# Kernel tuning notes

Measured on AMD Instinct MI355X. Metric: run time of the kernel, lower is better.

The kernel has to match this reference:

```python
import jax, jax.numpy as jnp
import numpy as np

BN_EPS = 1e-5

def _bn_eval(x, g, b, m, v):
    # BatchNorm1d in eval mode with running stats
    return (x - m) * (g / jnp.sqrt(v + BN_EPS)) + b

def _gcn_layer(x, adj, w, b):
    # D^-0.5 A D^-0.5 (X W) + b  (same math as diag(d^-0.5) @ adj @ diag(d^-0.5))
    deg = adj.sum(axis=1)
    dis = deg ** -0.5
    xw = x @ w
    return dis[:, None] * (adj @ (dis[:, None] * xw)) + b

def setup_inputs() -> dict:
    key = jax.random.key(0)
    ks = jax.random.split(key, 8)
    N, F, E, H, G, C = 16384, 1024, 256, 256, 128, 10
    def xavier(k, i, o):
        s = float(np.sqrt(6.0 / (i + o)))
        return jax.random.uniform(k, (i, o), jnp.float32, -s, s)
    return {
        "feature": jax.random.uniform(ks[0], (N, F), jnp.float32),
        "adj": jax.random.uniform(ks[1], (N, N), jnp.float32),
        "enc_w1": xavier(ks[2], F, 512), "enc_b1": jnp.zeros((512,), jnp.float32),
        "bn1_g": jnp.ones((512,), jnp.float32), "bn1_b": jnp.zeros((512,), jnp.float32),
        "bn1_m": jnp.zeros((512,), jnp.float32), "bn1_v": jnp.ones((512,), jnp.float32),
        "enc_w2": xavier(ks[3], 512, E), "enc_b2": jnp.zeros((E,), jnp.float32),
        "bn2_g": jnp.ones((E,), jnp.float32), "bn2_b": jnp.zeros((E,), jnp.float32),
        "bn2_m": jnp.zeros((E,), jnp.float32), "bn2_v": jnp.ones((E,), jnp.float32),
        "gcn1_w": xavier(ks[4], E, H), "gcn1_b": jnp.zeros((H,), jnp.float32),
        "gcn2_w": xavier(ks[5], H, G), "gcn2_b": jnp.zeros((G,), jnp.float32),
        "cls_w": xavier(ks[6], G, C), "cls_b": jnp.zeros((C,), jnp.float32),
    }

def reference(feature, adj, enc_w1, enc_b1, bn1_g, bn1_b, bn1_m, bn1_v,
              enc_w2, enc_b2, bn2_g, bn2_b, bn2_m, bn2_v,
              gcn1_w, gcn1_b, gcn2_w, gcn2_b, cls_w, cls_b):
    # encoder.encode (eval: dropout off, BN running stats)
    h = jax.nn.relu(_bn_eval(feature @ enc_w1 + enc_b1, bn1_g, bn1_b, bn1_m, bn1_v))
    h = jax.nn.relu(_bn_eval(h @ enc_w2 + enc_b2, bn2_g, bn2_b, bn2_m, bn2_v))
    h = jax.nn.relu(_gcn_layer(h, adj, gcn1_w, gcn1_b))
    h = jax.nn.relu(_gcn_layer(h, adj, gcn2_w, gcn2_b))
    out = jax.nn.sigmoid(h @ cls_w + cls_b)
    return jnp.clip(out, 1e-10, 1 - 1e-10)
```

## Files before the change

### kernel.cpp

```cpp
#include <hip/hip_runtime.h>
#include <stdint.h>

typedef unsigned short u16;
typedef unsigned int u32;
typedef __attribute__((ext_vector_type(4))) float f32x4;
typedef __attribute__((ext_vector_type(16))) float f32x16;
typedef __attribute__((ext_vector_type(8))) short s16x8;
typedef __attribute__((ext_vector_type(4))) short s16x4;
typedef __attribute__((ext_vector_type(2))) unsigned int u32x2;
typedef __attribute__((ext_vector_type(4))) unsigned int u32x4;
typedef __attribute__((ext_vector_type(8))) int i32x8;

__device__ __forceinline__ u16 f2bf(float x){
  unsigned u = __builtin_bit_cast(unsigned, x);
  u += 0x7fffu + ((u >> 16) & 1u);
  return (u16)(u >> 16);
}
__device__ __forceinline__ float bf2f(u16 b){
  return __builtin_bit_cast(float, (unsigned)b << 16);
}
__device__ __forceinline__ u32 pk_fp8x4(float a, float b, float c, float d){
  int w = 0;
  w = __builtin_amdgcn_cvt_pk_fp8_f32(a, b, w, false);
  w = __builtin_amdgcn_cvt_pk_fp8_f32(c, d, w, true);
  return (u32)w;
}


__device__ __forceinline__ void tcvtT_dev(const float* __restrict__ src, u16* __restrict__ dst,
                                          int K, int N, int bx, int by, char* smem){
  float (*t)[33] = (float (*)[33])smem;
  int tx = threadIdx.x & 31, ty = threadIdx.x >> 5;
  int n0 = bx * 32, k0 = by * 32;
  #pragma unroll
  for (int i = 0; i < 4; i++)
    t[ty + 8 * i][tx] = src[(size_t)(k0 + ty + 8 * i) * N + n0 + tx];
  __syncthreads();
  #pragma unroll
  for (int i = 0; i < 4; i++)
    dst[(size_t)(n0 + ty + 8 * i) * K + k0 + tx] = f2bf(t[tx][ty + 8 * i]);
}

__device__ __forceinline__ void bn_dev(const float* __restrict__ g, const float* __restrict__ b,
                                       const float* __restrict__ m, const float* __restrict__ v,
                                       const float* __restrict__ lin_b,
                                       float* __restrict__ s, float* __restrict__ bb,
                                       int n, int blk){
  int i = blk * 256 + threadIdx.x;
  if (i < n){
    float sc = g[i] * rsqrtf(v[i] + 1e-5f);
    s[i] = sc;
    bb[i] = (lin_b[i] - m[i]) * sc + b[i];
  }
}

__global__ __launch_bounds__(256) void prep0_kernel(
    const float* __restrict__ enc_w1, u16* __restrict__ w1t,
    const float* __restrict__ g, const float* __restrict__ b,
    const float* __restrict__ m, const float* __restrict__ v,
    const float* __restrict__ lin_b, float* __restrict__ s1, float* __restrict__ bb1)
{
  __shared__ char smem[32 * 33 * 4 + 64];
  if (blockIdx.x < 512)
    tcvtT_dev(enc_w1, w1t, 1024, 512, blockIdx.x & 15, blockIdx.x >> 4, smem);
  else
    bn_dev(g, b, m, v, lin_b, s1, bb1, 512, blockIdx.x - 512);
}

__global__ __launch_bounds__(256) void enc1_deg_kernel(
    const float* __restrict__ feature, const u16* __restrict__ w1t,
    u16* __restrict__ h1, const float* __restrict__ cs, const float* __restrict__ cb,
    const float* __restrict__ adj, unsigned char* __restrict__ adj8,
    float* __restrict__ dis,
    const float* __restrict__ enc_w2, u16* __restrict__ w2t,
    const float* __restrict__ gcn1_w, u16* __restrict__ g1t,
    const float* __restrict__ gcn2_w, u16* __restrict__ g2t,
    const float* __restrict__ bn2_g, const float* __restrict__ bn2_b,
    const float* __restrict__ bn2_m, const float* __restrict__ bn2_v,
    const float* __restrict__ enc_b2, float* __restrict__ s2, float* __restrict__ bb2)
{
  constexpr int BM = 128, BN = 256, BK = 64, WM = 2, WN = 2;
  constexpr int N = 512, K = 1024, NADJ = 16384;
  constexpr int WTM = BM / WM, WTN = BN / WN, FM = WTM / 16, FN = WTN / 16;
  constexpr int AIT = (BM * BK) / (256 * 4);
  constexpr int BIT = (BN * BK) / (256 * 8);

  __shared__ __align__(16) char smem[BM * BK * 2 + BN * BK * 2];

  if (blockIdx.x >= 16640){
    int p = blockIdx.x - 16640;
    if (p < 128)       tcvtT_dev(enc_w2, w2t, 512, 256, p & 7, p >> 3, smem);
    else if (p < 192){ int l = p - 128; tcvtT_dev(gcn1_w, g1t, 256, 256, l & 7, l >> 3, smem); }
    else if (p < 224){ int l = p - 192; tcvtT_dev(gcn2_w, g2t, 256, 128, l & 3, l >> 2, smem); }
    else               bn_dev(bn2_g, bn2_b, bn2_m, bn2_v, enc_b2, s2, bb2, 256, 0);
    return;
  }

  if (blockIdx.x >= 256){
    int row = blockIdx.x - 256;
    const float* rp = adj + (size_t)row * NADJ;
    unsigned char* wp = adj8 + (size_t)row * NADJ;
    float s = 0.f;
    #pragma unroll
    for (int it = 0; it < 4; ++it){
      const float* p = rp + it * 4096 + threadIdx.x * 16;
      f32x4 v[4];
      #pragma unroll
      for (int j = 0; j < 4; ++j) v[j] = *(const f32x4*)(p + 4 * j);
      u32x4 o;
      #pragma unroll
      for (int j = 0; j < 4; ++j){
        s += (v[j][0] + v[j][1]) + (v[j][2] + v[j][3]);
        o[j] = pk_fp8x4(v[j][0], v[j][1], v[j][2], v[j][3]);
      }
      *(u32x4*)(wp + it * 4096 + threadIdx.x * 16) = o;
    }
    #pragma unroll
    for (int d = 32; d > 0; d >>= 1) s += __shfl_down(s, d, 64);
    float* ps = (float*)smem;
    if ((threadIdx.x & 63) == 0) ps[threadIdx.x >> 6] = s;
    __syncthreads();
    if (threadIdx.x == 0) dis[row] = rsqrtf((ps[0] + ps[1]) + (ps[2] + ps[3]));
    return;
  }

  u16* As = (u16*)smem;
  u16* Bs = (u16*)(smem + BM * BK * 2);
  const int tid = threadIdx.x;
  const int lane = tid & 63;
  const int wid = tid >> 6;
  const int wr = wid / WN;
  const int wc = wid % WN;
  const int bm = (blockIdx.x & 127) * BM;
  const int bn = (blockIdx.x >> 7) * BN;

  f32x4 arf[AIT];
  s16x8 brb[BIT];

  auto load_tiles = [&](int k0){
    #pragma unroll
    for (int i = 0; i < AIT; i++){
      int e = (i * 256 + tid) * 4; int r = e / BK, c = e % BK;
      arf[i] = *(const f32x4*)(feature + (size_t)(bm + r) * K + k0 + c);
    }
    #pragma unroll
    for (int i = 0; i < BIT; i++){
      int e = (i * 256 + tid) * 8; int r = e / BK, c = e % BK;
      brb[i] = *(const s16x8*)(w1t + (size_t)(bn + r) * K + k0 + c);
    }
  };
  auto store_tiles = [&](){
    char* Ac = (char*)As; char* Bc = (char*)Bs;
    #pragma unroll
    for (int i = 0; i < AIT; i++){
      int e = (i * 256 + tid) * 4; int r = e / BK, c = e % BK;
      int off = ((r * BK + c) * 2) ^ ((r & 7) << 4);
      s16x4 o;
      o[0] = (short)f2bf(arf[i][0]); o[1] = (short)f2bf(arf[i][1]);
      o[2] = (short)f2bf(arf[i][2]); o[3] = (short)f2bf(arf[i][3]);
      *(s16x4*)(Ac + off) = o;
    }
    #pragma unroll
    for (int i = 0; i < BIT; i++){
      int e = (i * 256 + tid) * 8; int r = e / BK, c = e % BK;
      int off = ((r * BK + c) * 2) ^ ((r & 7) << 4);
      *(s16x8*)(Bc + off) = brb[i];
    }
  };

  f32x4 acc[FM][FN];
  #pragma unroll
  for (int m = 0; m < FM; m++)
    #pragma unroll
    for (int n = 0; n < FN; n++)
      acc[m][n] = (f32x4){0.f, 0.f, 0.f, 0.f};

  const int arow0 = wr * WTM + (lane & 15);
  const int brow0 = wc * WTN + (lane & 15);
  const int kof = (lane >> 4) * 8;

  load_tiles(0);
  for (int kt = 0; kt < K / BK; ++kt){
    __syncthreads();
    store_tiles();
    __syncthreads();
    if (kt + 1 < K / BK) load_tiles((kt + 1) * BK);
    const char* Ac = (const char*)As;
    const char* Bc = (const char*)Bs;
    #pragma unroll
    for (int ks = 0; ks < BK / 32; ++ks){
      s16x8 af[FM], bfr[FN];
      #pragma unroll
      for (int m = 0; m < FM; m++){
        int r = arow0 + m * 16;
        af[m] = *(const s16x8*)(Ac + (((r * BK + ks * 32 + kof) * 2) ^ ((r & 7) << 4)));
      }
      #pragma unroll
      for (int n = 0; n < FN; n++){
        int r = brow0 + n * 16;
        bfr[n] = *(const s16x8*)(Bc + (((r * BK + ks * 32 + kof) * 2) ^ ((r & 7) << 4)));
      }
      #pragma unroll
      for (int m = 0; m < FM; m++)
        #pragma unroll
        for (int n = 0; n < FN; n++)
          acc[m][n] = __builtin_amdgcn_mfma_f32_16x16x32_bf16(af[m], bfr[n], acc[m][n], 0, 0, 0);
    }
  }
  #pragma unroll
  for (int m = 0; m < FM; m++){
    #pragma unroll
    for (int n = 0; n < FN; n++){
      int col = bn + wc * WTN + n * 16 + (lane & 15);
      int row0 = bm + wr * WTM + m * 16 + (lane >> 4) * 4;
      #pragma unroll
      for (int r4 = 0; r4 < 4; r4++){
        float vv = fmaxf(acc[m][n][r4] * cs[col] + cb[col], 0.f);
        h1[(size_t)(row0 + r4) * N + col] = f2bf(vv);
      }
    }
  }
}

__global__ __launch_bounds__(512, 1)
void h2tT_kernel(const u16* __restrict__ h1, const u16* __restrict__ w2t,
                 const float* __restrict__ s2, const float* __restrict__ bb2,
                 const u16* __restrict__ g1t, const float* __restrict__ dis,
                 unsigned char* __restrict__ tT)
{
  constexpr int M = 16384, K1 = 512, K2 = 256, BK = 128;
  constexpr float SC = 256.f;

  __shared__ u16 As[64 * BK];
  __shared__ u16 Bs[256 * BK];
  __shared__ u16 H2s[64 * 256];

  const int tid = threadIdx.x;
  const int lane = tid & 63;
  const int wid = tid >> 6;
  const int wr = wid >> 2;
  const int wc = wid & 3;
  const int bm = blockIdx.x * 64;
  const int kof = (lane >> 4) * 8;

  {
    s16x8 arb[2], brb[8];
    auto load1 = [&](int k0){
      #pragma unroll
      for (int i = 0; i < 2; i++){
        int e = (i * 512 + tid) * 8; int r = e >> 7, c = e & 127;
        arb[i] = *(const s16x8*)(h1 + (size_t)(bm + r) * K1 + k0 + c);
      }
      #pragma unroll
      for (int i = 0; i < 8; i++){
        int e = (i * 512 + tid) * 8; int r = e >> 7, c = e & 127;
        brb[i] = *(const s16x8*)(w2t + (size_t)r * K1 + k0 + c);
      }
    };
    auto store1 = [&](){
      char* Ac = (char*)As; char* Bc = (char*)Bs;
      #pragma unroll
      for (int i = 0; i < 2; i++){
        int e = (i * 512 + tid) * 8; int r = e >> 7, c = e & 127;
        *(s16x8*)(Ac + (((r * BK + c) * 2) ^ ((r & 7) << 4))) = arb[i];
      }
      #pragma unroll
      for (int i = 0; i < 8; i++){
        int e = (i * 512 + tid) * 8; int r = e >> 7, c = e & 127;
        *(s16x8*)(Bc + (((r * BK + c) * 2) ^ ((r & 7) << 4))) = brb[i];
      }
    };

    f32x4 acc[2][4];
    #pragma unroll
    for (int m = 0; m < 2; m++)
      #pragma unroll
      for (int n = 0; n < 4; n++)
        acc[m][n] = (f32x4){0.f, 0.f, 0.f, 0.f};

    load1(0);
    for (int kt = 0; kt < K1 / BK; ++kt){
      __syncthreads();
      store1();
      __syncthreads();
      if (kt + 1 < K1 / BK) load1((kt + 1) * BK);
      const char* Ac = (const char*)As;
      const char* Bc = (const char*)Bs;
      #pragma unroll
      for (int ks = 0; ks < 4; ++ks){
        s16x8 af[2], bfr[4];
        #pragma unroll
        for (int m = 0; m < 2; m++){
          int r = wr * 32 + m * 16 + (lane & 15);
          af[m] = *(const s16x8*)(Ac + (((r * BK + ks * 32 + kof) * 2) ^ ((r & 7) << 4)));
        }
        #pragma unroll
        for (int n = 0; n < 4; n++){
          int r = wc * 64 + n * 16 + (lane & 15);
          bfr[n] = *(const s16x8*)(Bc + (((r * BK + ks * 32 + kof) * 2) ^ ((r & 7) << 4)));
        }
        #pragma unroll
        for (int m = 0; m < 2; m++)
          #pragma unroll
          for (int n = 0; n < 4; n++)
            acc[m][n] = __builtin_amdgcn_mfma_f32_16x16x32_bf16(af[m], bfr[n], acc[m][n], 0, 0, 0);
      }
    }
    __syncthreads();
    char* Hc = (char*)H2s;
    #pragma unroll
    for (int m = 0; m < 2; m++){
      #pragma unroll
      for (int n = 0; n < 4; n++){
        int col = wc * 64 + n * 16 + (lane & 15);
        int row0 = wr * 32 + m * 16 + (lane >> 4) * 4;
        #pragma unroll
        for (int r4 = 0; r4 < 4; r4++){
          int row = row0 + r4;
          float vv = fmaxf(acc[m][n][r4] * s2[col] + bb2[col], 0.f);
          *(u16*)(Hc + (((row * 256 + col) * 2) ^ ((row & 7) << 4))) = f2bf(vv);
        }
      }
    }
  }

  {
    s16x8 brb[8];
    auto load2 = [&](int k0){
      #pragma unroll
      for (int i = 0; i < 8; i++){
        int e = (i * 512 + tid) * 8; int r = e >> 7, c = e & 127;
        brb[i] = *(const s16x8*)(g1t + (size_t)r * K2 + k0 + c);
      }
    };
    auto store2 = [&](){
      char* Bc = (char*)Bs;
      #pragma unroll
      for (int i = 0; i < 8; i++){
        int e = (i * 512 + tid) * 8; int r = e >> 7, c = e & 127;
        *(s16x8*)(Bc + (((r * BK + c) * 2) ^ ((r & 7) << 4))) = brb[i];
      }
    };

    f32x4 acc[2][4];
    #pragma unroll
    for (int m = 0; m < 2; m++)
      #pragma unroll
      for (int n = 0; n < 4; n++)
        acc[m][n] = (f32x4){0.f, 0.f, 0.f, 0.f};

    load2(0);
    for (int kt = 0; kt < K2 / BK; ++kt){
      __syncthreads();
      store2();
      __syncthreads();
      if (kt + 1 < K2 / BK) load2((kt + 1) * BK);
      const char* Hc = (const char*)H2s;
      const char* Bc = (const char*)Bs;
      #pragma unroll
      for (int ks = 0; ks < 4; ++ks){
        s16x8 af[2], bfr[4];
        #pragma unroll
        for (int m = 0; m < 2; m++){
          int r = wr * 32 + m * 16 + (lane & 15);
          af[m] = *(const s16x8*)(Hc + (((r * 256 + kt * 128 + ks * 32 + kof) * 2) ^ ((r & 7) << 4)));
        }
        #pragma unroll
        for (int n = 0; n < 4; n++){
          int r = wc * 64 + n * 16 + (lane & 15);
          bfr[n] = *(const s16x8*)(Bc + (((r * BK + ks * 32 + kof) * 2) ^ ((r & 7) << 4)));
        }
        #pragma unroll
        for (int m = 0; m < 2; m++)
          #pragma unroll
          for (int n = 0; n < 4; n++)
            acc[m][n] = __builtin_amdgcn_mfma_f32_16x16x32_bf16(af[m], bfr[n], acc[m][n], 0, 0, 0);
      }
    }
    #pragma unroll
    for (int m = 0; m < 2; m++){
      #pragma unroll
      for (int n = 0; n < 4; n++){
        int col = wc * 64 + n * 16 + (lane & 15);
        int row0 = bm + wr * 32 + m * 16 + (lane >> 4) * 4;
        float v0 = acc[m][n][0] * dis[row0 + 0] * SC;
        float v1 = acc[m][n][1] * dis[row0 + 1] * SC;
        float v2 = acc[m][n][2] * dis[row0 + 2] * SC;
        float v3 = acc[m][n][3] * dis[row0 + 3] * SC;
        *(u32*)(tT + (size_t)col * M + row0) = pk_fp8x4(v0, v1, v2, v3);
      }
    }
  }
}

template<int BM, int BN>
__global__ __launch_bounds__(512, 1)
void gemm_mx(const unsigned char* __restrict__ A8, const unsigned char* __restrict__ B8,
             float* __restrict__ P, int M, int N, int K, int Ksub)
{
  constexpr int BK = 128;
  constexpr int AT = BM * BK;
  constexpr int BT = BN * BK;
  constexpr int AIT = AT / (512 * 16);
  constexpr int BIT = BT / (512 * 16);
  constexpr int NL = AIT + BIT;
  constexpr int WM = 2, WN = 4;
  constexpr int WTM = BM / WM;
  constexpr int WTN = BN / WN;
  constexpr int FM = WTM / 32;
  constexpr int FN = WTN / 32;
  static_assert(AIT >= 1 && BIT >= 1, "staging");

  __shared__ __align__(16) char LDS[3 * (AT + BT)];

  const int tid = threadIdx.x;
  const int lane = tid & 63;
  const int wid = tid >> 6;
  const int wr = wid >> 2;
  const int wc = wid & 3;
  const int bm = blockIdx.x * BM;
  const int kz = blockIdx.z * Ksub;

  auto stage = [&](int buf, int k0){
    char* ab = LDS + buf * (AT + BT);
    #pragma unroll
    for (int i = 0; i < AIT; i++){
      int e = (i * 512 + tid) * 16;
      int r = e >> 7, c = e & 127;
      int cc = c ^ ((r & 7) << 4);
      const unsigned char* g = A8 + (size_t)(bm + r) * K + k0 + cc;
      __builtin_amdgcn_global_load_lds((const __attribute__((address_space(1))) unsigned int*)g,
          (__attribute__((address_space(3))) unsigned int*)(ab + e), 16, 0, 0);
    }
    char* bb = ab + AT;
    #pragma unroll
    for (int i = 0; i < BIT; i++){
      int e = (i * 512 + tid) * 16;
      int r = e >> 7, c = e & 127;
      int cc = c ^ ((r & 7) << 4);
      const unsigned char* g = B8 + (size_t)r * K + k0 + cc;
      __builtin_amdgcn_global_load_lds((const __attribute__((address_space(1))) unsigned int*)g,
          (__attribute__((address_space(3))) unsigned int*)(bb + e), 16, 0, 0);
    }
  };

  f32x16 acc[FM][FN];
  #pragma unroll
  for (int m = 0; m < FM; m++)
    #pragma unroll
    for (int n = 0; n < FN; n++)
      #pragma unroll
      for (int i = 0; i < 16; i++)
        acc[m][n][i] = 0.f;

  const int nk = Ksub / BK;
  stage(0, kz);
  stage(1, kz + BK);
  for (int kt = 0; kt < nk; ++kt){
    if (kt + 1 < nk) asm volatile("s_waitcnt vmcnt(%0)" :: "n"(NL) : "memory");
    else             asm volatile("s_waitcnt vmcnt(0)" ::: "memory");
    __builtin_amdgcn_s_barrier();
    if (kt + 2 < nk) stage((kt + 2) % 3, kz + (kt + 2) * BK);
    const char* ab = LDS + (kt % 3) * (AT + BT);
    const char* bb = ab + AT;
    #pragma unroll
    for (int ks = 0; ks < 2; ks++){
      const int c0 = ks * 64 + (lane >> 5) * 32;
      i32x8 af[FM], bf_[FN];
      #pragma unroll
      for (int m = 0; m < FM; m++){
        int r = wr * WTM + m * 32 + (lane & 31);
        int sw = (r & 7) << 4;
        int o = r * BK + c0;
        u32x4 lo = *(const u32x4*)(ab + (o ^ sw));
        u32x4 hi = *(const u32x4*)(ab + ((o + 16) ^ sw));
        af[m][0] = lo[0]; af[m][1] = lo[1]; af[m][2] = lo[2]; af[m][3] = lo[3];
        af[m][4] = hi[0]; af[m][5] = hi[1]; af[m][6] = hi[2]; af[m][7] = hi[3];
      }
      #pragma unroll
      for (int n = 0; n < FN; n++){
        int r = wc * WTN + n * 32 + (lane & 31);
        int sw = (r & 7) << 4;
        int o = r * BK + c0;
        u32x4 lo = *(const u32x4*)(bb + (o ^ sw));
        u32x4 hi = *(const u32x4*)(bb + ((o + 16) ^ sw));
        bf_[n][0] = lo[0]; bf_[n][1] = lo[1]; bf_[n][2] = lo[2]; bf_[n][3] = lo[3];
        bf_[n][4] = hi[0]; bf_[n][5] = hi[1]; bf_[n][6] = hi[2]; bf_[n][7] = hi[3];
      }
      #pragma unroll
      for (int m = 0; m < FM; m++)
        #pragma unroll
        for (int n = 0; n < FN; n++)
          acc[m][n] = __builtin_amdgcn_mfma_scale_f32_32x32x64_f8f6f4(
              af[m], bf_[n], acc[m][n], 0, 0, 0, 0x7F7F7F7F, 0, 0x7F7F7F7F);
    }
  }

  float* Pz = P + (size_t)blockIdx.z * M * N;
  #pragma unroll
  for (int m = 0; m < FM; m++){
    #pragma unroll
    for (int n = 0; n < FN; n++){
      int colg = wc * WTN + n * 32 + (lane & 31);
      int rbase = bm + wr * WTM + m * 32 + (lane >> 5) * 4;
      #pragma unroll
      for (int i = 0; i < 16; i++){
        int rowg = rbase + (i & 3) + 8 * (i >> 2);
        Pz[(size_t)rowg * N + colg] = acc[m][n][i];
      }
    }
  }
}

__global__ __launch_bounds__(256, 1)
void t2g_kernel(const float* __restrict__ part, const float* __restrict__ dis,
                const float* __restrict__ g1b, const u16* __restrict__ g2t,
                unsigned char* __restrict__ t2T)
{
  constexpr int M = 16384, H = 256, BK = 64;
  constexpr float SC = 256.f, SCI = 1.f / 256.f;
  const size_t MN = (size_t)M * H;

  __shared__ u16 As[64 * BK];
  __shared__ u16 Bs[128 * BK];

  const int tid = threadIdx.x;
  const int lane = tid & 63;
  const int wid = tid >> 6;
  const int wr = wid >> 1;
  const int wc = wid & 1;
  const int bm = blockIdx.x * 64;
  const int kof = (lane >> 4) * 8;

  f32x4 a0r[4], a1r[4], gbr[4];
  float dsr[4];
  s16x8 brb[4];

  auto load_tiles = [&](int k0){
    #pragma unroll
    for (int i = 0; i < 4; i++){
      int e = (i * 256 + tid) * 4; int r = e >> 6, c = e & 63;
      size_t pi = (size_t)(bm + r) * H + k0 + c;
      a0r[i] = *(const f32x4*)(part + pi);
      a1r[i] = *(const f32x4*)(part + MN + pi);
      gbr[i] = *(const f32x4*)(g1b + k0 + c);
      dsr[i] = dis[bm + r];
    }
    #pragma unroll
    for (int i = 0; i < 4; i++){
      int e = (i * 256 + tid) * 8; int r = e >> 6, c = e & 63;
      brb[i] = *(const s16x8*)(g2t + (size_t)r * H + k0 + c);
    }
  };
  auto store_tiles = [&](){
    char* Ac = (char*)As; char* Bc = (char*)Bs;
    #pragma unroll
    for (int i = 0; i < 4; i++){
      int e = (i * 256 + tid) * 4; int r = e >> 6, c = e & 63;
      float dsc = dsr[i] * SCI;
      s16x4 o;
      #pragma unroll
      for (int j = 0; j < 4; j++){
        float vv = fmaxf(dsc * (a0r[i][j] + a1r[i][j]) + gbr[i][j], 0.f);
        o[j] = (short)f2bf(vv);
      }
      *(s16x4*)(Ac + (((r * BK + c) * 2) ^ ((r & 7) << 4))) = o;
    }
    #pragma unroll
    for (int i = 0; i < 4; i++){
      int e = (i * 256 + tid) * 8; int r = e >> 6, c = e & 63;
      *(s16x8*)(Bc + (((r * BK + c) * 2) ^ ((r & 7) << 4))) = brb[i];
    }
  };

  f32x4 acc[2][4];
  #pragma unroll
  for (int m = 0; m < 2; m++)
    #pragma unroll
    for (int n = 0; n < 4; n++)
      acc[m][n] = (f32x4){0.f, 0.f, 0.f, 0.f};

  load_tiles(0);
  for (int kt = 0; kt < H / BK; ++kt){
    __syncthreads();
    store_tiles();
    __syncthreads();
    if (kt + 1 < H / BK) load_tiles((kt + 1) * BK);
    const char* Ac = (const char*)As;
    const char* Bc = (const char*)Bs;
    #pragma unroll
    for (int ks = 0; ks < 2; ++ks){
      s16x8 af[2], bfr[4];
      #pragma unroll
      for (int m = 0; m < 2; m++){
        int r = wr * 32 + m * 16 + (lane & 15);
        af[m] = *(const s16x8*)(Ac + (((r * BK + ks * 32 + kof) * 2) ^ ((r & 7) << 4)));
      }
      #pragma unroll
      for (int n = 0; n < 4; n++){
        int r = wc * 64 + n * 16 + (lane & 15);
        bfr[n] = *(const s16x8*)(Bc + (((r * BK + ks * 32 + kof) * 2) ^ ((r & 7) << 4)));
      }
      #pragma unroll
      for (int m = 0; m < 2; m++)
        #pragma unroll
        for (int n = 0; n < 4; n++)
          acc[m][n] = __builtin_amdgcn_mfma_f32_16x16x32_bf16(af[m], bfr[n], acc[m][n], 0, 0, 0);
    }
  }

  #pragma unroll
  for (int m = 0; m < 2; m++){
    #pragma unroll
    for (int n = 0; n < 4; n++){
      int col = wc * 64 + n * 16 + (lane & 15);
      int row0 = bm + wr * 32 + m * 16 + (lane >> 4) * 4;
      float v0 = acc[m][n][0] * dis[row0 + 0] * SC;
      float v1 = acc[m][n][1] * dis[row0 + 1] * SC;
      float v2 = acc[m][n][2] * dis[row0 + 2] * SC;
      float v3 = acc[m][n][3] * dis[row0 + 3] * SC;
      *(u32*)(t2T + (size_t)col * M + row0) = pk_fp8x4(v0, v1, v2, v3);
    }
  }
}

__global__ __launch_bounds__(256) void cls2_kernel(const float* __restrict__ part,
                                                   const float* __restrict__ dis,
                                                   const float* __restrict__ g2b,
                                                   const float* __restrict__ w,
                                                   const float* __restrict__ b,
                                                   float* __restrict__ out)
{
  constexpr int M = 16384, G = 128;
  constexpr float SCI = 1.f / 256.f;
  const size_t MN = (size_t)M * G;
  __shared__ float ws_[G * 10];
  __shared__ float bs_[10];
  __shared__ float gb_[G];
  for (int i = threadIdx.x; i < G * 10; i += 256) ws_[i] = w[i];
  if (threadIdx.x < 10) bs_[threadIdx.x] = b[threadIdx.x];
  if (threadIdx.x < G) gb_[threadIdx.x] = g2b[threadIdx.x];
  __syncthreads();
  int row = blockIdx.x * 256 + threadIdx.x;
  const float* p0 = part + (size_t)row * G;
  const float* p1 = p0 + MN;
  float dr = dis[row] * SCI;
  float acc[10];
  #pragma unroll
  for (int c = 0; c < 10; c++) acc[c] = bs_[c];
  for (int k16 = 0; k16 < G; k16 += 16){
    f32x4 a0[4], a1[4];
    #pragma unroll
    for (int j = 0; j < 4; j++){
      a0[j] = *(const f32x4*)(p0 + k16 + 4 * j);
      a1[j] = *(const f32x4*)(p1 + k16 + 4 * j);
    }
    #pragma unroll
    for (int j = 0; j < 16; j++){
      float h = fmaxf(dr * (a0[j >> 2][j & 3] + a1[j >> 2][j & 3]) + gb_[k16 + j], 0.f);
      #pragma unroll
      for (int c = 0; c < 10; c++) acc[c] = fmaf(h, ws_[(k16 + j) * 10 + c], acc[c]);
    }
  }
  #pragma unroll
  for (int c = 0; c < 10; c++){
    float sg = 1.f / (1.f + expf(-acc[c]));
    sg = fminf(fmaxf(sg, 1e-10f), 1.f - 1e-10f);
    out[(size_t)row * 10 + c] = sg;
  }
}


extern "C" void kernel_launch(void* const* d_in, const int* in_sizes, int n_in,
                              void* d_out, int out_size, void* d_ws, size_t ws_size,
                              hipStream_t stream)
{
  (void)in_sizes; (void)n_in; (void)out_size; (void)ws_size;
  const float* feature = (const float*)d_in[0];
  const float* adj     = (const float*)d_in[1];
  const float* enc_w1  = (const float*)d_in[2];
  const float* enc_b1  = (const float*)d_in[3];
  const float* bn1_g   = (const float*)d_in[4];
  const float* bn1_b   = (const float*)d_in[5];
  const float* bn1_m   = (const float*)d_in[6];
  const float* bn1_v   = (const float*)d_in[7];
  const float* enc_w2  = (const float*)d_in[8];
  const float* enc_b2  = (const float*)d_in[9];
  const float* bn2_g   = (const float*)d_in[10];
  const float* bn2_b   = (const float*)d_in[11];
  const float* bn2_m   = (const float*)d_in[12];
  const float* bn2_v   = (const float*)d_in[13];
  const float* gcn1_w  = (const float*)d_in[14];
  const float* gcn1_b  = (const float*)d_in[15];
  const float* gcn2_w  = (const float*)d_in[16];
  const float* gcn2_b  = (const float*)d_in[17];
  const float* cls_w   = (const float*)d_in[18];
  const float* cls_b   = (const float*)d_in[19];
  float* out = (float*)d_out;

  const int NN = 16384, F = 1024, H1 = 512, E = 256, H = 256, G = 128;

  char* ws = (char*)d_ws;
  size_t off = 0;
  auto alloc = [&](size_t bytes) -> char* {
    char* p = ws + off; off += (bytes + 255) & ~(size_t)255; return p;
  };
  float* dis = (float*)alloc((size_t)NN * 4);
  float* s1  = (float*)alloc((size_t)H1 * 4);
  float* bb1 = (float*)alloc((size_t)H1 * 4);
  float* s2  = (float*)alloc((size_t)E * 4);
  float* bb2 = (float*)alloc((size_t)E * 4);
  u16* w1t = (u16*)alloc((size_t)H1 * F * 2);
  u16* w2t = (u16*)alloc((size_t)E * H1 * 2);
  u16* g1t = (u16*)alloc((size_t)H * E * 2);
  u16* g2t = (u16*)alloc((size_t)G * H * 2);
  u16* h1  = (u16*)alloc((size_t)NN * H1 * 2);
  unsigned char* tT  = (unsigned char*)alloc((size_t)E * NN);
  unsigned char* t2T = (unsigned char*)alloc((size_t)G * NN);
  float* part = (float*)alloc((size_t)2 * NN * H * 4);
  unsigned char* adj8 = (unsigned char*)alloc((size_t)NN * NN);

  prep0_kernel<<<514, 256, 0, stream>>>(enc_w1, w1t, bn1_g, bn1_b, bn1_m, bn1_v, enc_b1, s1, bb1);

  enc1_deg_kernel<<<256 + NN + 225, 256, 0, stream>>>(
      feature, w1t, h1, s1, bb1, adj, adj8, dis,
      enc_w2, w2t, gcn1_w, g1t, gcn2_w, g2t,
      bn2_g, bn2_b, bn2_m, bn2_v, enc_b2, s2, bb2);

  h2tT_kernel<<<NN / 64, 512, 0, stream>>>(h1, w2t, s2, bb2, g1t, dis, tT);

  gemm_mx<128,256><<<dim3(NN/128, 1, 2), 512, 0, stream>>>(
      adj8, tT, part, NN, H, NN, NN/2);

  t2g_kernel<<<NN / 64, 256, 0, stream>>>(part, dis, gcn1_b, g2t, t2T);

  gemm_mx<128,128><<<dim3(NN/128, 1, 2), 512, 0, stream>>>(
      adj8, t2T, part, NN, G, NN, NN/2);

  cls2_kernel<<<NN / 256, 256, 0, stream>>>(part, dis, gcn2_b, cls_w, cls_b, out);
}
```

Baseline: 472.2 us.

## Quantize adjacency to FP4 and use FP4xFP8 scaled MFMA for GCN aggregation

Adjacency is quantized to 4-bit FP4 (e2m1 with a block scale of 2^-2) instead of FP8, halving the bytes of the cached adjacency copy and of the A-operand traffic in both aggregation GEMMs. The GEMM kernel is rewritten to stage packed nibbles with a new LDS swizzle and feed the scaled f8f6f4 MFMA in FP4 mode. The second GEMM's split-K is raised to 4 ways, and the classifier kernel now sums four partials. The cost is coarser adjacency precision, and the part buffer is still sized for only 2*N*H floats. Four partials of N*G floats equal exactly that size, so it fits.

```diff
diff --git a/kernel.cpp b/kernel.cpp
--- a/kernel.cpp
+++ b/kernel.cpp
@@ -24,6 +24,11 @@
   w = __builtin_amdgcn_cvt_pk_fp8_f32(a, b, w, false);
   w = __builtin_amdgcn_cvt_pk_fp8_f32(c, d, w, true);
   return (u32)w;
+}
+__device__ __forceinline__ u32 q_fp4(float v){
+  float s4 = v * 4.f;
+  float rq = (s4 < 2.f) ? rintf(s4 + s4) : (rintf(s4) + 2.f);
+  return (u32)(int)rq;
 }
 
 
@@ -70,7 +75,7 @@
 __global__ __launch_bounds__(256) void enc1_deg_kernel(
     const float* __restrict__ feature, const u16* __restrict__ w1t,
     u16* __restrict__ h1, const float* __restrict__ cs, const float* __restrict__ cb,
-    const float* __restrict__ adj, unsigned char* __restrict__ adj8,
+    const float* __restrict__ adj, unsigned char* __restrict__ adj4,
     float* __restrict__ dis,
     const float* __restrict__ enc_w2, u16* __restrict__ w2t,
     const float* __restrict__ gcn1_w, u16* __restrict__ g1t,
@@ -99,7 +104,7 @@
   if (blockIdx.x >= 256){
     int row = blockIdx.x - 256;
     const float* rp = adj + (size_t)row * NADJ;
-    unsigned char* wp = adj8 + (size_t)row * NADJ;
+    unsigned char* wp = adj4 + (size_t)row * (NADJ >> 1);
     float s = 0.f;
     #pragma unroll
     for (int it = 0; it < 4; ++it){
@@ -107,13 +112,19 @@
       f32x4 v[4];
       #pragma unroll
       for (int j = 0; j < 4; ++j) v[j] = *(const f32x4*)(p + 4 * j);
-      u32x4 o;
+      u32 w0 = 0, w1 = 0;
       #pragma unroll
       for (int j = 0; j < 4; ++j){
         s += (v[j][0] + v[j][1]) + (v[j][2] + v[j][3]);
-        o[j] = pk_fp8x4(v[j][0], v[j][1], v[j][2], v[j][3]);
-      }
-      *(u32x4*)(wp + it * 4096 + threadIdx.x * 16) = o;
+        #pragma unroll
+        for (int q = 0; q < 4; ++q){
+          u32 c = q_fp4(v[j][q]);
+          int idx = j * 4 + q;
+          if (idx < 8) w0 |= c << (4 * idx);
+          else         w1 |= c << (4 * (idx - 8));
+        }
+      }
+      *(u32x2*)(wp + it * 2048 + threadIdx.x * 8) = (u32x2){w0, w1};
     }
     #pragma unroll
     for (int d = 32; d > 0; d >>= 1) s += __shfl_down(s, d, 64);
@@ -393,25 +404,20 @@
   }
 }
 
-template<int BM, int BN>
+template<int BN>
 __global__ __launch_bounds__(512, 1)
-void gemm_mx(const unsigned char* __restrict__ A8, const unsigned char* __restrict__ B8,
-             float* __restrict__ P, int M, int N, int K, int Ksub)
+void gemm_mx4(const unsigned char* __restrict__ A4, const unsigned char* __restrict__ B8,
+              float* __restrict__ P, int M, int N, int K, int Ksub)
 {
-  constexpr int BK = 128;
-  constexpr int AT = BM * BK;
-  constexpr int BT = BN * BK;
-  constexpr int AIT = AT / (512 * 16);
-  constexpr int BIT = BT / (512 * 16);
-  constexpr int NL = AIT + BIT;
-  constexpr int WM = 2, WN = 4;
-  constexpr int WTM = BM / WM;
-  constexpr int WTN = BN / WN;
-  constexpr int FM = WTM / 32;
+  constexpr int BM = 128, BK = 128;
+  constexpr int ATB = BM * (BK / 2);
+  constexpr int BTB = BN * BK;
+  constexpr int BIT = BTB / (512 * 16);
+  constexpr int NL = 1 + BIT;
+  constexpr int WTN = BN / 4;
   constexpr int FN = WTN / 32;
-  static_assert(AIT >= 1 && BIT >= 1, "staging");
-
-  __shared__ __align__(16) char LDS[3 * (AT + BT)];
+
+  __shared__ __align__(16) char LDS[3 * (ATB + BTB)];
 
   const int tid = threadIdx.x;
   const int lane = tid & 63;
@@ -422,17 +428,19 @@
   const int kz = blockIdx.z * Ksub;
 
   auto stage = [&](int buf, int k0){
-    char* ab = LDS + buf * (AT + BT);
-    #pragma unroll
-    for (int i = 0; i < AIT; i++){
-      int e = (i * 512 + tid) * 16;
-      int r = e >> 7, c = e & 127;
-      int cc = c ^ ((r & 7) << 4);
-      const unsigned char* g = A8 + (size_t)(bm + r) * K + k0 + cc;
+    char* ab = LDS + buf * (ATB + BTB);
+    {
+      int e = tid * 16;
+      int j = e >> 7, off = e & 127;
+      int h = ((off >> 6) ^ (j >> 1)) & 1;
+      int t = off ^ (h << 4) ^ ((j & 3) << 5);
+      int kb = t & 63;
+      int r = 2 * j + h;
+      const unsigned char* g = A4 + (size_t)(bm + r) * (K >> 1) + (k0 >> 1) + kb;
       __builtin_amdgcn_global_load_lds((const __attribute__((address_space(1))) unsigned int*)g,
           (__attribute__((address_space(3))) unsigned int*)(ab + e), 16, 0, 0);
     }
-    char* bb = ab + AT;
+    char* bb = ab + ATB;
     #pragma unroll
     for (int i = 0; i < BIT; i++){
       int e = (i * 512 + tid) * 16;
@@ -444,9 +452,9 @@
     }
   };
 
-  f32x16 acc[FM][FN];
-  #pragma unroll
-  for (int m = 0; m < FM; m++)
+  f32x16 acc[2][FN];
+  #pragma unroll
+  for (int m = 0; m < 2; m++)
     #pragma unroll
     for (int n = 0; n < FN; n++)
       #pragma unroll
@@ -461,21 +469,20 @@
     else             asm volatile("s_waitcnt vmcnt(0)" ::: "memory");
     __builtin_amdgcn_s_barrier();
     if (kt + 2 < nk) stage((kt + 2) % 3, kz + (kt + 2) * BK);
-    const char* ab = LDS + (kt % 3) * (AT + BT);
-    const char* bb = ab + AT;
+    const char* ab = LDS + (kt % 3) * (ATB + BTB);
+    const char* bb = ab + ATB;
     #pragma unroll
     for (int ks = 0; ks < 2; ks++){
       const int c0 = ks * 64 + (lane >> 5) * 32;
-      i32x8 af[FM], bf_[FN];
-      #pragma unroll
-      for (int m = 0; m < FM; m++){
-        int r = wr * WTM + m * 32 + (lane & 31);
-        int sw = (r & 7) << 4;
-        int o = r * BK + c0;
-        u32x4 lo = *(const u32x4*)(ab + (o ^ sw));
-        u32x4 hi = *(const u32x4*)(ab + ((o + 16) ^ sw));
+      const int kb = c0 >> 1;
+      i32x8 af[2], bf_[FN];
+      #pragma unroll
+      for (int m = 0; m < 2; m++){
+        int r = wr * 64 + m * 32 + (lane & 31);
+        int adr = ((r >> 1) << 7) + ((((r & 1) << 6) | kb) ^ ((r & 7) << 4));
+        u32x4 lo = *(const u32x4*)(ab + adr);
         af[m][0] = lo[0]; af[m][1] = lo[1]; af[m][2] = lo[2]; af[m][3] = lo[3];
-        af[m][4] = hi[0]; af[m][5] = hi[1]; af[m][6] = hi[2]; af[m][7] = hi[3];
+        af[m][4] = 0; af[m][5] = 0; af[m][6] = 0; af[m][7] = 0;
       }
       #pragma unroll
       for (int n = 0; n < FN; n++){
@@ -488,21 +495,22 @@
         bf_[n][4] = hi[0]; bf_[n][5] = hi[1]; bf_[n][6] = hi[2]; bf_[n][7] = hi[3];
       }
       #pragma unroll
-      for (int m = 0; m < FM; m++)
+      for (int m = 0; m < 2; m++)
         #pragma unroll
         for (int n = 0; n < FN; n++)
           acc[m][n] = __builtin_amdgcn_mfma_scale_f32_32x32x64_f8f6f4(
-              af[m], bf_[n], acc[m][n], 0, 0, 0, 0x7F7F7F7F, 0, 0x7F7F7F7F);
+              af[m], bf_[n], acc[m][n], 4 , 0 ,
+              0, 0x7D7D7D7D , 0, 0x7F7F7F7F );
     }
   }
 
   float* Pz = P + (size_t)blockIdx.z * M * N;
   #pragma unroll
-  for (int m = 0; m < FM; m++){
+  for (int m = 0; m < 2; m++){
     #pragma unroll
     for (int n = 0; n < FN; n++){
       int colg = wc * WTN + n * 32 + (lane & 31);
-      int rbase = bm + wr * WTM + m * 32 + (lane >> 5) * 4;
+      int rbase = bm + wr * 64 + m * 32 + (lane >> 5) * 4;
       #pragma unroll
       for (int i = 0; i < 16; i++){
         int rowg = rbase + (i & 3) + 8 * (i >> 2);
@@ -643,21 +651,22 @@
   __syncthreads();
   int row = blockIdx.x * 256 + threadIdx.x;
   const float* p0 = part + (size_t)row * G;
-  const float* p1 = p0 + MN;
   float dr = dis[row] * SCI;
   float acc[10];
   #pragma unroll
   for (int c = 0; c < 10; c++) acc[c] = bs_[c];
   for (int k16 = 0; k16 < G; k16 += 16){
-    f32x4 a0[4], a1[4];
+    f32x4 a[4];
     #pragma unroll
     for (int j = 0; j < 4; j++){
-      a0[j] = *(const f32x4*)(p0 + k16 + 4 * j);
-      a1[j] = *(const f32x4*)(p1 + k16 + 4 * j);
+      a[j] = *(const f32x4*)(p0 + k16 + 4 * j);
+      a[j] += *(const f32x4*)(p0 + MN + k16 + 4 * j);
+      a[j] += *(const f32x4*)(p0 + 2 * MN + k16 + 4 * j);
+      a[j] += *(const f32x4*)(p0 + 3 * MN + k16 + 4 * j);
     }
     #pragma unroll
     for (int j = 0; j < 16; j++){
-      float h = fmaxf(dr * (a0[j >> 2][j & 3] + a1[j >> 2][j & 3]) + gb_[k16 + j], 0.f);
+      float h = fmaxf(dr * a[j >> 2][j & 3] + gb_[k16 + j], 0.f);
       #pragma unroll
       for (int c = 0; c < 10; c++) acc[c] = fmaf(h, ws_[(k16 + j) * 10 + c], acc[c]);
     }
@@ -718,24 +727,24 @@
   unsigned char* tT  = (unsigned char*)alloc((size_t)E * NN);
   unsigned char* t2T = (unsigned char*)alloc((size_t)G * NN);
   float* part = (float*)alloc((size_t)2 * NN * H * 4);
-  unsigned char* adj8 = (unsigned char*)alloc((size_t)NN * NN);
+  unsigned char* adj4 = (unsigned char*)alloc((size_t)NN * NN / 2);
 
   prep0_kernel<<<514, 256, 0, stream>>>(enc_w1, w1t, bn1_g, bn1_b, bn1_m, bn1_v, enc_b1, s1, bb1);
 
   enc1_deg_kernel<<<256 + NN + 225, 256, 0, stream>>>(
-      feature, w1t, h1, s1, bb1, adj, adj8, dis,
+      feature, w1t, h1, s1, bb1, adj, adj4, dis,
       enc_w2, w2t, gcn1_w, g1t, gcn2_w, g2t,
       bn2_g, bn2_b, bn2_m, bn2_v, enc_b2, s2, bb2);
 
   h2tT_kernel<<<NN / 64, 512, 0, stream>>>(h1, w2t, s2, bb2, g1t, dis, tT);
 
-  gemm_mx<128,256><<<dim3(NN/128, 1, 2), 512, 0, stream>>>(
-      adj8, tT, part, NN, H, NN, NN/2);
+  gemm_mx4<256><<<dim3(NN/128, 1, 2), 512, 0, stream>>>(
+      adj4, tT, part, NN, H, NN, NN/2);
 
   t2g_kernel<<<NN / 64, 256, 0, stream>>>(part, dis, gcn1_b, g2t, t2T);
 
-  gemm_mx<128,128><<<dim3(NN/128, 1, 2), 512, 0, stream>>>(
-      adj8, t2T, part, NN, G, NN, NN/2);
+  gemm_mx4<128><<<dim3(NN/128, 1, 4), 512, 0, stream>>>(
+      adj4, t2T, part, NN, G, NN, NN/4);
 
   cls2_kernel<<<NN / 256, 256, 0, stream>>>(part, dis, gcn2_b, cls_w, cls_b, out);
 }
```

Result: slower. 508.6 us (+7.7%).
